# Performance work log

Hardware: AMD Instinct MI355X
Metric: run time of the kernel (lower is better)

## Reference

```python
import jax, jax.numpy as jnp
import numpy as np

N, E, B, D = 50000, 1600000, 256, 64


def _lin(k, fan_in, fan_out):
    kw, kb = jax.random.split(k)
    bound = 1.0 / np.sqrt(fan_in)
    w = jax.random.uniform(kw, (fan_in, fan_out), jnp.float32, -bound, bound)
    b = jax.random.uniform(kb, (fan_out,), jnp.float32, -bound, bound)
    return w, b


def setup_inputs() -> dict:
    key = jax.random.key(0)
    ks = jax.random.split(key, 16)
    inp = {
        "x": jax.random.normal(ks[0], (N, D), jnp.float32),
        "edge_attr": jax.random.normal(ks[1], (E, D), jnp.float32),
        "u": jax.random.normal(ks[2], (B, D), jnp.float32),
        "edge_index": jax.random.randint(ks[3], (2, E), 0, N, jnp.int32),
        "batch": jnp.sort(jax.random.randint(ks[4], (N,), 0, B, jnp.int32)),
    }
    # three MLPs: edge (in 4D), node (in 3D), global (in 3D); dims [2D, 2D, D]
    specs = [("e", 4 * D), ("n", 3 * D), ("g", 3 * D)]
    ki = 5
    for name, in_dim in specs:
        dims = [in_dim, 2 * D, 2 * D, D]
        for li in range(3):
            w, b = _lin(ks[ki], dims[li], dims[li + 1]); ki += 1
            inp[f"{name}w{li+1}"] = w
            inp[f"{name}b{li+1}"] = b
    return inp


def _mlp(h, w1, b1, w2, b2, w3, b3):
    h = h @ w1 + b1
    h = jax.nn.relu(h) @ w2 + b2
    h = jax.nn.relu(h) @ w3 + b3
    return h


def _scatter_mean(src, idx, num_segments):
    s = jax.ops.segment_sum(src, idx, num_segments=num_segments)
    c = jax.ops.segment_sum(jnp.ones_like(src[:, :1]), idx, num_segments=num_segments)
    return s / jnp.maximum(c, 1.0)


def reference(x, edge_attr, u,
              ew1, eb1, ew2, eb2, ew3, eb3,
              nw1, nb1, nw2, nb2, nw3, nb3,
              gw1, gb1, gw2, gb2, gw3, gb3,
              edge_index, batch):
    row, col = edge_index[0], edge_index[1]
    # edge model: cat[src, dest, edge_attr, u[batch[row]]] -> MLP
    e_in = jnp.concatenate([x[row], x[col], edge_attr, u[batch[row]]], axis=1)  # [E, 4D]
    e = _mlp(e_in, ew1, eb1, ew2, eb2, ew3, eb3)  # [E, D]
    # node model: scatter_mean(edge_attr', row) cat x cat u[batch] -> MLP
    n_agg = _scatter_mean(e, row, x.shape[0])  # [N, D]
    n_in = jnp.concatenate([n_agg, x, u[batch]], axis=1)  # [N, 3D]
    xn = _mlp(n_in, nw1, nb1, nw2, nb2, nw3, nb3)  # [N, D]
    # global model: cat[u, scatter_mean(x', batch), scatter_mean(e', batch[row])]
    edge_mean = _scatter_mean(e, batch[row], u.shape[0])  # [B, D]
    node_mean = _scatter_mean(xn, batch, u.shape[0])  # [B, D]
    g_in = jnp.concatenate([u, node_mean, edge_mean], axis=1)  # [B, 3D]
    un = _mlp(g_in, gw1, gb1, gw2, gb2, gw3, gb3)  # [B, D]
    return xn, e, un
```

## Files before the change

### kernel.cpp

```cpp
#include <hip/hip_runtime.h>

#define NN 50000
#define EE 1600000
#define BBATCH 256
#define DD 64

typedef _Float16 f16;
typedef _Float16 f16x4 __attribute__((ext_vector_type(4)));
typedef _Float16 f16x8 __attribute__((ext_vector_type(8)));
typedef float f32x4 __attribute__((ext_vector_type(4)));

#define MFMA16(a,b,c) __builtin_amdgcn_mfma_f32_16x16x32_f16((a),(b),(c),0,0,0)

constexpr int EW1_RL  = 264;
constexpr int EW1_OFF = 0;
constexpr int EW2_OFF = EW1_OFF + 128 * EW1_RL;
constexpr int EW3_OFF = EW2_OFF + 128 * 136;
constexpr int EH_OFF  = EW3_OFF + 64 * 136;
constexpr int EB_OFF  = EH_OFF + 8 * 16 * 72;
constexpr int ELDS    = EB_OFF + 640;

constexpr int NW1_RL  = 200;
constexpr int NW1_OFF = 0;
constexpr int NW2_OFF = NW1_OFF + 128 * NW1_RL;
constexpr int NW3_OFF = NW2_OFF + 128 * 136;
constexpr int NH_OFF  = NW3_OFF + 64 * 136;
constexpr int NB_OFF  = NH_OFF + 4 * 32 * 136;
constexpr int NLDS    = NB_OFF + 640;

__device__ __forceinline__ f16x8 pack8(const float* __restrict__ p) {
  f32x4 a = *(const f32x4*)p;
  f32x4 b = *(const f32x4*)(p + 4);
  f16x8 r;
  r[0]=(f16)a[0]; r[1]=(f16)a[1]; r[2]=(f16)a[2]; r[3]=(f16)a[3];
  r[4]=(f16)b[0]; r[5]=(f16)b[1]; r[6]=(f16)b[2]; r[7]=(f16)b[3];
  return r;
}
__device__ __forceinline__ f16x8 pack8s(const float* __restrict__ p, float sc) {
  f32x4 a = *(const f32x4*)p;
  f32x4 b = *(const f32x4*)(p + 4);
  a = a * sc; b = b * sc;
  f16x8 r;
  r[0]=(f16)a[0]; r[1]=(f16)a[1]; r[2]=(f16)a[2]; r[3]=(f16)a[3];
  r[4]=(f16)b[0]; r[5]=(f16)b[1]; r[6]=(f16)b[2]; r[7]=(f16)b[3];
  return r;
}
__device__ __forceinline__ f16x8 cvt8(f32x4 a, f32x4 b) {
  f16x8 r;
  r[0]=(f16)a[0]; r[1]=(f16)a[1]; r[2]=(f16)a[2]; r[3]=(f16)a[3];
  r[4]=(f16)b[0]; r[5]=(f16)b[1]; r[6]=(f16)b[2]; r[7]=(f16)b[3];
  return r;
}

template<int KSL, int W1RL, int W1O, int W2O, int W3O>
__device__ __forceinline__ void mlp3_core(f16* __restrict__ sm,
    const float* __restrict__ b1l, const float* __restrict__ b2l,
    const float* __restrict__ b3l,
    const f16x8 (&A1)[2][KSL], const int hb, const int r15, const int g,
    f32x4 (&acc3)[2][4])
{
  #pragma unroll
  for (int hh = 0; hh < 2; ++hh) {
    f32x4 acc[2][4];
    #pragma unroll
    for (int nt = 0; nt < 4; ++nt) {
      const float bv = b1l[(hh*4 + nt)*16 + r15];
      acc[0][nt] = (f32x4){bv, bv, bv, bv};
      acc[1][nt] = acc[0][nt];
    }
    #pragma unroll
    for (int s = 0; s < KSL; ++s) {
      #pragma unroll
      for (int nt = 0; nt < 4; ++nt) {
        const f16x8 bf = *(const f16x8*)&sm[W1O + ((hh*4+nt)*16 + r15) * W1RL + s*32 + g*8];
        acc[0][nt] = MFMA16(A1[0][s], bf, acc[0][nt]);
        acc[1][nt] = MFMA16(A1[1][s], bf, acc[1][nt]);
      }
    }
    #pragma unroll
    for (int mt = 0; mt < 2; ++mt)
      #pragma unroll
      for (int nt = 0; nt < 4; ++nt)
        #pragma unroll
        for (int i = 0; i < 4; ++i)
          sm[hb + (mt*16 + g*4 + i)*136 + (hh*4+nt)*16 + r15] =
              (f16)fmaxf(acc[mt][nt][i], 0.f);
  }

  f16x8 A2[2][4];
  #pragma unroll
  for (int mt = 0; mt < 2; ++mt)
    #pragma unroll
    for (int s = 0; s < 4; ++s)
      A2[mt][s] = *(const f16x8*)&sm[hb + (mt*16 + r15)*136 + s*32 + g*8];

  #pragma unroll
  for (int hh = 0; hh < 2; ++hh) {
    f32x4 acc[2][4];
    #pragma unroll
    for (int nt = 0; nt < 4; ++nt) {
      const float bv = b2l[(hh*4 + nt)*16 + r15];
      acc[0][nt] = (f32x4){bv, bv, bv, bv};
      acc[1][nt] = acc[0][nt];
    }
    #pragma unroll
    for (int s = 0; s < 4; ++s) {
      #pragma unroll
      for (int nt = 0; nt < 4; ++nt) {
        const f16x8 bf = *(const f16x8*)&sm[W2O + ((hh*4+nt)*16 + r15)*136 + s*32 + g*8];
        acc[0][nt] = MFMA16(A2[0][s], bf, acc[0][nt]);
        acc[1][nt] = MFMA16(A2[1][s], bf, acc[1][nt]);
      }
    }
    #pragma unroll
    for (int mt = 0; mt < 2; ++mt)
      #pragma unroll
      for (int nt = 0; nt < 4; ++nt)
        #pragma unroll
        for (int i = 0; i < 4; ++i)
          sm[hb + (mt*16 + g*4 + i)*136 + (hh*4+nt)*16 + r15] =
              (f16)fmaxf(acc[mt][nt][i], 0.f);
  }

  f16x8 A3[2][4];
  #pragma unroll
  for (int mt = 0; mt < 2; ++mt)
    #pragma unroll
    for (int s = 0; s < 4; ++s)
      A3[mt][s] = *(const f16x8*)&sm[hb + (mt*16 + r15)*136 + s*32 + g*8];

  #pragma unroll
  for (int nt = 0; nt < 4; ++nt) {
    const float bv = b3l[nt*16 + r15];
    acc3[0][nt] = (f32x4){bv, bv, bv, bv};
    acc3[1][nt] = acc3[0][nt];
  }
  #pragma unroll
  for (int s = 0; s < 4; ++s) {
    #pragma unroll
    for (int nt = 0; nt < 4; ++nt) {
      const f16x8 bf = *(const f16x8*)&sm[W3O + (nt*16 + r15)*136 + s*32 + g*8];
      acc3[0][nt] = MFMA16(A3[0][s], bf, acc3[0][nt]);
      acc3[1][nt] = MFMA16(A3[1][s], bf, acc3[1][nt]);
    }
  }
}

__global__ void transpose_all(
    const float* __restrict__ e1, const float* __restrict__ e2, const float* __restrict__ e3,
    const float* __restrict__ n1, const float* __restrict__ n2, const float* __restrict__ n3,
    const float* __restrict__ q1, const float* __restrict__ q2, const float* __restrict__ q3,
    f16* __restrict__ dst) {
  int tid = blockIdx.x * 256 + threadIdx.x;
  const int o1=32768,o2=49152,o3=57344,o4=81920,o5=98304,o6=106496,o7=131072,o8=147456,o9=155648;
  if (tid >= o9) return;
  const float* src; int in, od, rel;
  if      (tid < o1) { src=e1; in=256; od=128; rel=tid;    }
  else if (tid < o2) { src=e2; in=128; od=128; rel=tid-o1; }
  else if (tid < o3) { src=e3; in=128; od=64;  rel=tid-o2; }
  else if (tid < o4) { src=n1; in=192; od=128; rel=tid-o3; }
  else if (tid < o5) { src=n2; in=128; od=128; rel=tid-o4; }
  else if (tid < o6) { src=n3; in=128; od=64;  rel=tid-o5; }
  else if (tid < o7) { src=q1; in=192; od=128; rel=tid-o6; }
  else if (tid < o8) { src=q2; in=128; od=128; rel=tid-o7; }
  else               { src=q3; in=128; od=64;  rel=tid-o8; }
  int o = rel / in, i = rel - o * in;
  dst[tid] = (f16)src[(size_t)i * od + o];
}

__global__ void cvt_xu(const float* __restrict__ x, const float* __restrict__ u,
                       f16* __restrict__ xh, f16* __restrict__ uh) {
  const int XT = NN * 64 / 4;
  const int UT = BBATCH * 64 / 4;
  int tid = blockIdx.x * 256 + threadIdx.x;
  for (int i = tid; i < XT; i += gridDim.x * 256) {
    f32x4 v = *(const f32x4*)&x[(size_t)i * 4];
    f16x4 h; h[0]=(f16)v[0]; h[1]=(f16)v[1]; h[2]=(f16)v[2]; h[3]=(f16)v[3];
    *(f16x4*)&xh[(size_t)i * 4] = h;
  }
  if (tid < UT) {
    f32x4 v = *(const f32x4*)&u[(size_t)tid * 4];
    f16x4 h; h[0]=(f16)v[0]; h[1]=(f16)v[1]; h[2]=(f16)v[2]; h[3]=(f16)v[3];
    *(f16x4*)&uh[(size_t)tid * 4] = h;
  }
}

__global__ void count_kernel(const int* __restrict__ ei, int* __restrict__ deg) {
  int tid = blockIdx.x * 256 + threadIdx.x;
  if (tid < EE) atomicAdd(&deg[ei[tid]], 1);
}

__global__ __launch_bounds__(1024) void scan_kernel(const int* __restrict__ deg,
                                                    int* __restrict__ offs,
                                                    int* __restrict__ cursor) {
  const int t = threadIdx.x;
  const int per = (NN + 1023) / 1024;
  const int s0 = t * per;
  int s1 = s0 + per; if (s1 > NN) s1 = NN;
  int sum = 0;
  for (int i = s0; i < s1; ++i) sum += deg[i];
  const int lane = t & 63, wid = t >> 6;
  int v = sum;
  #pragma unroll
  for (int off = 1; off < 64; off <<= 1) {
    int o = __shfl_up(v, off);
    if (lane >= off) v += o;
  }
  __shared__ int wsums[16];
  __shared__ int wexcl[16];
  if (lane == 63) wsums[wid] = v;
  __syncthreads();
  if (t == 0) { int run = 0; for (int k = 0; k < 16; ++k) { wexcl[k] = run; run += wsums[k]; } }
  __syncthreads();
  int run = wexcl[wid] + v - sum;
  for (int i = s0; i < s1; ++i) { int d = deg[i]; offs[i] = run; cursor[i] = run; run += d; }
  if (t == 1023) offs[NN] = run;
}

__global__ void fill_kernel(const int* __restrict__ ei, int* __restrict__ cursor,
                            int* __restrict__ elist) {
  int tid = blockIdx.x * 256 + threadIdx.x;
  if (tid < EE) {
    int r = ei[tid];
    int pos = atomicAdd(&cursor[r], 1);
    elist[pos] = tid;
  }
}

__global__ __launch_bounds__(512, 2) void edge_mlp_kernel(
    const f16* __restrict__ xh, const float* __restrict__ ea,
    const f16* __restrict__ uh, const int* __restrict__ ei,
    const int* __restrict__ batch,
    const f16* __restrict__ w1t, const f16* __restrict__ w2t, const f16* __restrict__ w3t,
    const float* __restrict__ b1, const float* __restrict__ b2, const float* __restrict__ b3,
    float* __restrict__ e_out)
{
  __shared__ __align__(16) f16 sm[ELDS];
  const int t = threadIdx.x;
  for (int c = t; c < 4096; c += 512) { int r = c >> 5, kc = c & 31;
    *(uint4*)&sm[EW1_OFF + r*EW1_RL + kc*8] = *(const uint4*)&w1t[r*256 + kc*8]; }
  for (int c = t; c < 2048; c += 512) { int r = c >> 4, kc = c & 15;
    *(uint4*)&sm[EW2_OFF + r*136 + kc*8] = *(const uint4*)&w2t[r*128 + kc*8]; }
  for (int c = t; c < 1024; c += 512) { int r = c >> 4, kc = c & 15;
    *(uint4*)&sm[EW3_OFF + r*136 + kc*8] = *(const uint4*)&w3t[r*128 + kc*8]; }
  float* bias = (float*)&sm[EB_OFF];
  if (t < 128) { bias[t] = b1[t]; bias[128 + t] = b2[t]; }
  else if (t < 192) { bias[256 + (t - 128)] = b3[t - 128]; }
  __syncthreads();

  const int l = t & 63, w = t >> 6;
  const int r15 = l & 15, g = l >> 4;
  const int hb = EH_OFF + w * (16 * 72);
  const int NT = EE / 256;
  const int stride = gridDim.x;
  const int t0 = blockIdx.x;

  int rC[2], cC[2], bC[2];
  int rN[2], cN[2], bN[2];
  f16x8 Bx[2][6];
  f32x4 Gea[2][2][2];

  auto issueXU = [&](const int (&rr)[2], const int (&cc)[2], const int (&bb)[2]) {
    #pragma unroll
    for (int mt = 0; mt < 2; ++mt) {
      const f16* pr = xh + (size_t)rr[mt] * 64 + g * 8;
      const f16* pc = xh + (size_t)cc[mt] * 64 + g * 8;
      const f16* pu = uh + (size_t)bb[mt] * 64 + g * 8;
      Bx[mt][0] = *(const f16x8*)pr;        Bx[mt][1] = *(const f16x8*)(pr + 32);
      Bx[mt][2] = *(const f16x8*)pc;        Bx[mt][3] = *(const f16x8*)(pc + 32);
      Bx[mt][4] = *(const f16x8*)pu;        Bx[mt][5] = *(const f16x8*)(pu + 32);
    }
  };
  auto issueEA = [&](int tt) {
    #pragma unroll
    for (int mt = 0; mt < 2; ++mt) {
      const float* pe = ea + ((size_t)(tt * 256 + w * 32 + mt * 16 + r15)) * 64 + g * 8;
      #pragma unroll
      for (int ss = 0; ss < 2; ++ss) {
        Gea[mt][ss][0] = *(const f32x4*)(pe + ss * 32);
        Gea[mt][ss][1] = *(const f32x4*)(pe + ss * 32 + 4);
      }
    }
  };

  {
    int rr[2], cc[2], bb[2];
    #pragma unroll
    for (int mt = 0; mt < 2; ++mt) {
      const int eid = t0 * 256 + w * 32 + mt * 16 + r15;
      rr[mt] = ei[eid]; cc[mt] = ei[EE + eid];
    }
    #pragma unroll
    for (int mt = 0; mt < 2; ++mt) bb[mt] = batch[rr[mt]];
    issueXU(rr, cc, bb); issueEA(t0);
    int t1 = t0 + stride; if (t1 >= NT) t1 = t0;
    #pragma unroll
    for (int mt = 0; mt < 2; ++mt) {
      const int eid = t1 * 256 + w * 32 + mt * 16 + r15;
      rC[mt] = ei[eid]; cC[mt] = ei[EE + eid];
    }
    #pragma unroll
    for (int mt = 0; mt < 2; ++mt) bC[mt] = batch[rC[mt]];
  }

  for (int tile = t0; tile < NT; tile += stride) {
    f16x8 A[2][8];
    #pragma unroll
    for (int mt = 0; mt < 2; ++mt) {
      A[mt][0] = Bx[mt][0]; A[mt][1] = Bx[mt][1];
      A[mt][2] = Bx[mt][2]; A[mt][3] = Bx[mt][3];
      A[mt][4] = cvt8(Gea[mt][0][0], Gea[mt][0][1]);
      A[mt][5] = cvt8(Gea[mt][1][0], Gea[mt][1][1]);
      A[mt][6] = Bx[mt][4]; A[mt][7] = Bx[mt][5];
    }

    int t2 = tile + 2 * stride; if (t2 >= NT) t2 = t0;
    #pragma unroll
    for (int mt = 0; mt < 2; ++mt) {
      const int eid = t2 * 256 + w * 32 + mt * 16 + r15;
      rN[mt] = ei[eid]; cN[mt] = ei[EE + eid];
    }

    f32x4 acc1[2][8];
    #pragma unroll
    for (int a = 0; a < 8; ++a) {
      const f32x4 bv = *(const f32x4*)&bias[a*16 + g*4];
      acc1[0][a] = bv; acc1[1][a] = bv;
    }
    #pragma unroll
    for (int s = 0; s < 8; ++s)
      #pragma unroll
      for (int a = 0; a < 8; ++a) {
        const f16x8 wf = *(const f16x8*)&sm[EW1_OFF + (a*16 + r15)*EW1_RL + s*32 + g*8];
        acc1[0][a] = MFMA16(wf, A[0][s], acc1[0][a]);
        acc1[1][a] = MFMA16(wf, A[1][s], acc1[1][a]);
      }

    #pragma unroll
    for (int mt = 0; mt < 2; ++mt) bN[mt] = batch[rN[mt]];

    f16x8 B2[2][4];
    #pragma unroll
    for (int mt = 0; mt < 2; ++mt)
      #pragma unroll
      for (int hh = 0; hh < 2; ++hh) {
        #pragma unroll
        for (int ap = 0; ap < 4; ++ap) {
          const f32x4 v = acc1[mt][hh*4 + ap];
          f16x4 hv;
          hv[0]=(f16)fmaxf(v[0],0.f); hv[1]=(f16)fmaxf(v[1],0.f);
          hv[2]=(f16)fmaxf(v[2],0.f); hv[3]=(f16)fmaxf(v[3],0.f);
          *(f16x4*)&sm[hb + r15*72 + ap*16 + g*4] = hv;
        }
        #pragma unroll
        for (int sl = 0; sl < 2; ++sl)
          B2[mt][hh*2 + sl] = *(const f16x8*)&sm[hb + r15*72 + sl*32 + g*8];
      }

    int t1 = tile + stride; if (t1 >= NT) t1 = t0;
    issueXU(rC, cC, bC);

    f32x4 acc2[2][8];
    #pragma unroll
    for (int a = 0; a < 8; ++a) {
      const f32x4 bv = *(const f32x4*)&bias[128 + a*16 + g*4];
      acc2[0][a] = bv; acc2[1][a] = bv;
    }
    #pragma unroll
    for (int s = 0; s < 4; ++s)
      #pragma unroll
      for (int a = 0; a < 8; ++a) {
        const f16x8 wf = *(const f16x8*)&sm[EW2_OFF + (a*16 + r15)*136 + s*32 + g*8];
        acc2[0][a] = MFMA16(wf, B2[0][s], acc2[0][a]);
        acc2[1][a] = MFMA16(wf, B2[1][s], acc2[1][a]);
      }

    f16x8 B3[2][4];
    #pragma unroll
    for (int mt = 0; mt < 2; ++mt)
      #pragma unroll
      for (int hh = 0; hh < 2; ++hh) {
        #pragma unroll
        for (int ap = 0; ap < 4; ++ap) {
          const f32x4 v = acc2[mt][hh*4 + ap];
          f16x4 hv;
          hv[0]=(f16)fmaxf(v[0],0.f); hv[1]=(f16)fmaxf(v[1],0.f);
          hv[2]=(f16)fmaxf(v[2],0.f); hv[3]=(f16)fmaxf(v[3],0.f);
          *(f16x4*)&sm[hb + r15*72 + ap*16 + g*4] = hv;
        }
        #pragma unroll
        for (int sl = 0; sl < 2; ++sl)
          B3[mt][hh*2 + sl] = *(const f16x8*)&sm[hb + r15*72 + sl*32 + g*8];
      }

    issueEA(t1);

    f32x4 acc3[2][4];
    #pragma unroll
    for (int a = 0; a < 4; ++a) {
      const f32x4 bv = *(const f32x4*)&bias[256 + a*16 + g*4];
      acc3[0][a] = bv; acc3[1][a] = bv;
    }
    #pragma unroll
    for (int s = 0; s < 4; ++s)
      #pragma unroll
      for (int a = 0; a < 4; ++a) {
        const f16x8 wf = *(const f16x8*)&sm[EW3_OFF + (a*16 + r15)*136 + s*32 + g*8];
        acc3[0][a] = MFMA16(wf, B3[0][s], acc3[0][a]);
        acc3[1][a] = MFMA16(wf, B3[1][s], acc3[1][a]);
      }

    const int base = tile * 256 + w * 32;
    #pragma unroll
    for (int mt = 0; mt < 2; ++mt) {
      const int m = base + mt * 16 + r15;
      #pragma unroll
      for (int a = 0; a < 4; ++a)
        *(f32x4*)&e_out[(size_t)m * 64 + a*16 + g*4] = acc3[mt][a];
    }

    #pragma unroll
    for (int mt = 0; mt < 2; ++mt) { rC[mt] = rN[mt]; cC[mt] = cN[mt]; bC[mt] = bN[mt]; }
  }
}

__global__ void nsum_kernel(const float* __restrict__ e_src, const int* __restrict__ offs,
                            const int* __restrict__ elist, float* __restrict__ n_sum) {
  const int l = threadIdx.x & 63;
  const int wid = (blockIdx.x * blockDim.x + threadIdx.x) >> 6;
  const int nw = (gridDim.x * blockDim.x) >> 6;
  for (int node = wid; node < NN; node += nw) {
    const int s = offs[node], e = offs[node + 1];
    float acc = 0.f;
    int j = s;
    for (; j + 8 <= e; j += 8) {
      float v0 = e_src[(size_t)elist[j]   * 64 + l];
      float v1 = e_src[(size_t)elist[j+1] * 64 + l];
      float v2 = e_src[(size_t)elist[j+2] * 64 + l];
      float v3 = e_src[(size_t)elist[j+3] * 64 + l];
      float v4 = e_src[(size_t)elist[j+4] * 64 + l];
      float v5 = e_src[(size_t)elist[j+5] * 64 + l];
      float v6 = e_src[(size_t)elist[j+6] * 64 + l];
      float v7 = e_src[(size_t)elist[j+7] * 64 + l];
      acc += ((v0 + v1) + (v2 + v3)) + ((v4 + v5) + (v6 + v7));
    }
    for (; j < e; ++j) acc += e_src[(size_t)elist[j] * 64 + l];
    n_sum[(size_t)node * 64 + l] = acc;
  }
}

__global__ __launch_bounds__(256, 1) void node_mlp_kernel(
    const float* __restrict__ x, const float* __restrict__ u,
    const int* __restrict__ batch, const float* __restrict__ n_sum,
    const int* __restrict__ deg,
    const f16* __restrict__ w1t, const f16* __restrict__ w2t, const f16* __restrict__ w3t,
    const float* __restrict__ b1, const float* __restrict__ b2, const float* __restrict__ b3,
    float* __restrict__ xn_out)
{
  __shared__ __align__(16) f16 sm[NLDS];
  const int t = threadIdx.x;
  for (int c = t; c < 3072; c += 256) { int r = c / 24, kc = c - r * 24;
    *(uint4*)&sm[NW1_OFF + r*NW1_RL + kc*8] = *(const uint4*)&w1t[r*192 + kc*8]; }
  for (int c = t; c < 2048; c += 256) { int r = c >> 4, kc = c & 15;
    *(uint4*)&sm[NW2_OFF + r*136 + kc*8] = *(const uint4*)&w2t[r*128 + kc*8]; }
  for (int c = t; c < 1024; c += 256) { int r = c >> 4, kc = c & 15;
    *(uint4*)&sm[NW3_OFF + r*136 + kc*8] = *(const uint4*)&w3t[r*128 + kc*8]; }
  float* bias = (float*)&sm[NB_OFF];
  if (t < 128) { bias[t] = b1[t]; bias[128 + t] = b2[t]; }
  if (t < 64)  { bias[256 + t] = b3[t]; }
  __syncthreads();

  const int l = t & 63, w = t >> 6;
  const int r15 = l & 15, g = l >> 4;
  const int hb = NH_OFF + w * (32 * 136);
  const int NTT = (NN + 127) / 128;

  for (int tile = blockIdx.x; tile < NTT; tile += gridDim.x) {
    const int base = tile * 128 + w * 32;
    f16x8 A1[2][6];
    #pragma unroll
    for (int mt = 0; mt < 2; ++mt) {
      int raw = base + mt * 16 + r15;
      int node = raw < NN ? raw : NN - 1;
      float inv = 1.0f / fmaxf((float)deg[node], 1.0f);
      const float* sA = n_sum + (size_t)node * 64;
      const float* sB = x + (size_t)node * 64;
      const float* sC = u + (size_t)batch[node] * 64;
      #pragma unroll
      for (int s = 0; s < 6; ++s) {
        const int off = (s & 1) * 32 + g * 8;
        if (s < 2)      A1[mt][s] = pack8s(sA + off, inv);
        else if (s < 4) A1[mt][s] = pack8(sB + off);
        else            A1[mt][s] = pack8(sC + off);
      }
    }
    f32x4 acc3[2][4];
    mlp3_core<6, NW1_RL, NW1_OFF, NW2_OFF, NW3_OFF>(sm, bias, bias + 128, bias + 256,
                                                    A1, hb, r15, g, acc3);
    #pragma unroll
    for (int mt = 0; mt < 2; ++mt)
      #pragma unroll
      for (int nt = 0; nt < 4; ++nt)
        #pragma unroll
        for (int i = 0; i < 4; ++i) {
          const int m = base + mt * 16 + g * 4 + i;
          if (m < NN) xn_out[(size_t)m * 64 + nt * 16 + r15] = acc3[mt][nt][i];
        }
  }
}

__global__ void bstart_kernel(const int* __restrict__ batch, int* __restrict__ bstart) {
  int tid = blockIdx.x * 256 + threadIdx.x;
  if (tid >= NN) return;
  int b = batch[tid];
  if (tid == 0) { for (int k = 0; k <= b; ++k) bstart[k] = 0; }
  else { int pb = batch[tid - 1]; for (int k = pb + 1; k <= b; ++k) bstart[k] = tid; }
  if (tid == NN - 1) { for (int k = b + 1; k <= BBATCH; ++k) bstart[k] = NN; }
}

__global__ void batch_sum_kernel(const float* __restrict__ xn, const float* __restrict__ n_sum,
                                 const int* __restrict__ deg, const int* __restrict__ bstart,
                                 float* __restrict__ nbsum, float* __restrict__ ebsum,
                                 int* __restrict__ ncnt, int* __restrict__ ecnt) {
  __shared__ float red0[256];
  __shared__ float red1[256];
  __shared__ int   redi[256];
  const int b = blockIdx.x;
  const int s = bstart[b], e = bstart[b + 1];
  const int t = threadIdx.x, c = t & 63, j0 = t >> 6;
  float xs = 0.f, ns = 0.f; int dc = 0;
  for (int j = s + j0; j < e; j += 4) {
    xs += xn[(size_t)j * 64 + c];
    ns += n_sum[(size_t)j * 64 + c];
    if (c == 0) dc += deg[j];
  }
  red0[t] = xs; red1[t] = ns; redi[t] = dc;
  __syncthreads();
  if (t < 128) { red0[t] += red0[t + 128]; red1[t] += red1[t + 128]; redi[t] += redi[t + 128]; }
  __syncthreads();
  if (t < 64) {
    float a0 = red0[t] + red0[t + 64];
    float a1 = red1[t] + red1[t + 64];
    nbsum[b * 64 + t] = a0;
    ebsum[b * 64 + t] = a1;
    if (t == 0) { ncnt[b] = e - s; ecnt[b] = redi[0] + redi[64]; }
  }
}

__global__ __launch_bounds__(256, 1) void global_mlp_kernel(
    const float* __restrict__ u, const float* __restrict__ nbsum,
    const float* __restrict__ ebsum, const int* __restrict__ ncnt,
    const int* __restrict__ ecnt,
    const f16* __restrict__ w1t, const f16* __restrict__ w2t, const f16* __restrict__ w3t,
    const float* __restrict__ b1, const float* __restrict__ b2, const float* __restrict__ b3,
    float* __restrict__ un_out)
{
  __shared__ __align__(16) f16 sm[NLDS];
  const int t = threadIdx.x;
  for (int c = t; c < 3072; c += 256) { int r = c / 24, kc = c - r * 24;
    *(uint4*)&sm[NW1_OFF + r*NW1_RL + kc*8] = *(const uint4*)&w1t[r*192 + kc*8]; }
  for (int c = t; c < 2048; c += 256) { int r = c >> 4, kc = c & 15;
    *(uint4*)&sm[NW2_OFF + r*136 + kc*8] = *(const uint4*)&w2t[r*128 + kc*8]; }
  for (int c = t; c < 1024; c += 256) { int r = c >> 4, kc = c & 15;
    *(uint4*)&sm[NW3_OFF + r*136 + kc*8] = *(const uint4*)&w3t[r*128 + kc*8]; }
  float* bias = (float*)&sm[NB_OFF];
  if (t < 128) { bias[t] = b1[t]; bias[128 + t] = b2[t]; }
  if (t < 64)  { bias[256 + t] = b3[t]; }
  __syncthreads();

  const int l = t & 63, w = t >> 6;
  const int r15 = l & 15, g = l >> 4;
  const int hb = NH_OFF + w * (32 * 136);
  const int base = blockIdx.x * 128 + w * 32;

  f16x8 A1[2][6];
  #pragma unroll
  for (int mt = 0; mt < 2; ++mt) {
    const int r = base + mt * 16 + r15;
    const float invn = 1.0f / fmaxf((float)ncnt[r], 1.0f);
    const float inve = 1.0f / fmaxf((float)ecnt[r], 1.0f);
    const float* sA = u + (size_t)r * 64;
    const float* sB = nbsum + (size_t)r * 64;
    const float* sC = ebsum + (size_t)r * 64;
    #pragma unroll
    for (int s = 0; s < 6; ++s) {
      const int off = (s & 1) * 32 + g * 8;
      if (s < 2)      A1[mt][s] = pack8(sA + off);
      else if (s < 4) A1[mt][s] = pack8s(sB + off, invn);
      else            A1[mt][s] = pack8s(sC + off, inve);
    }
  }
  f32x4 acc3[2][4];
  mlp3_core<6, NW1_RL, NW1_OFF, NW2_OFF, NW3_OFF>(sm, bias, bias + 128, bias + 256,
                                                  A1, hb, r15, g, acc3);
  #pragma unroll
  for (int mt = 0; mt < 2; ++mt)
    #pragma unroll
    for (int nt = 0; nt < 4; ++nt)
      #pragma unroll
      for (int i = 0; i < 4; ++i) {
        const int m = base + mt * 16 + g * 4 + i;
        un_out[(size_t)m * 64 + nt * 16 + r15] = acc3[mt][nt][i];
      }
}

extern "C" void kernel_launch(void* const* d_in, const int* in_sizes, int n_in,
                              void* d_out, int out_size, void* d_ws, size_t ws_size,
                              hipStream_t stream)
{
  (void)in_sizes; (void)n_in; (void)out_size; (void)ws_size;
  const float* x     = (const float*)d_in[0];
  const float* ea    = (const float*)d_in[1];
  const float* u     = (const float*)d_in[2];
  const int*   ei    = (const int*)d_in[3];
  const int*   batch = (const int*)d_in[4];
  const float* ew1 = (const float*)d_in[5];  const float* eb1 = (const float*)d_in[6];
  const float* ew2 = (const float*)d_in[7];  const float* eb2 = (const float*)d_in[8];
  const float* ew3 = (const float*)d_in[9];  const float* eb3 = (const float*)d_in[10];
  const float* nw1 = (const float*)d_in[11]; const float* nb1 = (const float*)d_in[12];
  const float* nw2 = (const float*)d_in[13]; const float* nb2 = (const float*)d_in[14];
  const float* nw3 = (const float*)d_in[15]; const float* nb3 = (const float*)d_in[16];
  const float* gw1 = (const float*)d_in[17]; const float* gb1 = (const float*)d_in[18];
  const float* gw2 = (const float*)d_in[19]; const float* gb2 = (const float*)d_in[20];
  const float* gw3 = (const float*)d_in[21]; const float* gb3 = (const float*)d_in[22];

  float* xn_out = (float*)d_out;
  float* e_out  = xn_out + (size_t)NN * DD;
  float* un_out = e_out + (size_t)EE * DD;

  char* p = (char*)d_ws;
  auto alloc = [&](size_t bytes) -> void* {
    void* r = (void*)p; p += (bytes + 255) & ~(size_t)255; return r;
  };
  f16* wtE1 = (f16*)alloc(256 * 128 * 2);
  f16* wtE2 = (f16*)alloc(128 * 128 * 2);
  f16* wtE3 = (f16*)alloc(128 * 64 * 2);
  f16* wtN1 = (f16*)alloc(192 * 128 * 2);
  f16* wtN2 = (f16*)alloc(128 * 128 * 2);
  f16* wtN3 = (f16*)alloc(128 * 64 * 2);
  f16* wtG1 = (f16*)alloc(192 * 128 * 2);
  f16* wtG2 = (f16*)alloc(128 * 128 * 2);
  f16* wtG3 = (f16*)alloc(128 * 64 * 2);
  int* deg    = (int*)alloc((size_t)NN * 4);
  int* offs   = (int*)alloc((size_t)(NN + 1) * 4);
  int* cursor = (int*)alloc((size_t)NN * 4);
  int* elist  = (int*)alloc((size_t)EE * 4);
  int* bstart = (int*)alloc((size_t)(BBATCH + 1) * 4);
  float* nbsum = (float*)alloc((size_t)BBATCH * 64 * 4);
  float* ebsum = (float*)alloc((size_t)BBATCH * 64 * 4);
  int* ncnt = (int*)alloc((size_t)BBATCH * 4);
  int* ecnt = (int*)alloc((size_t)BBATCH * 4);
  float* n_sum = (float*)alloc((size_t)NN * 64 * 4);
  f16* xh = (f16*)alloc((size_t)NN * 64 * 2);
  f16* uh = (f16*)alloc((size_t)BBATCH * 64 * 2);

  transpose_all<<<dim3(608), dim3(256), 0, stream>>>(
      ew1, ew2, ew3, nw1, nw2, nw3, gw1, gw2, gw3, wtE1);
  cvt_xu<<<dim3(1024), dim3(256), 0, stream>>>(x, u, xh, uh);

  hipMemsetAsync(deg, 0, (size_t)NN * 4, stream);
  count_kernel<<<dim3(6250), dim3(256), 0, stream>>>(ei, deg);
  scan_kernel<<<dim3(1), dim3(1024), 0, stream>>>(deg, offs, cursor);
  fill_kernel<<<dim3(6250), dim3(256), 0, stream>>>(ei, cursor, elist);

  edge_mlp_kernel<<<dim3(256), dim3(512), 0, stream>>>(
      xh, ea, uh, ei, batch, wtE1, wtE2, wtE3, eb1, eb2, eb3, e_out);

  nsum_kernel<<<dim3(2048), dim3(256), 0, stream>>>(e_out, offs, elist, n_sum);

  node_mlp_kernel<<<dim3(128), dim3(256), 0, stream>>>(
      x, u, batch, n_sum, deg, wtN1, wtN2, wtN3, nb1, nb2, nb3, xn_out);

  bstart_kernel<<<dim3((NN + 255) / 256), dim3(256), 0, stream>>>(batch, bstart);
  batch_sum_kernel<<<dim3(BBATCH), dim3(256), 0, stream>>>(
      xn_out, n_sum, deg, bstart, nbsum, ebsum, ncnt, ecnt);

  global_mlp_kernel<<<dim3(2), dim3(256), 0, stream>>>(
      u, nbsum, ebsum, ncnt, ecnt, wtG1, wtG2, wtG3, gb1, gb2, gb3, un_out);
}
```

Measured before the change: 752.8 us.

## Fuse prep kernels, unroll nsum gather to 16, double nsum and node grids

Merges the weight transpose, x/u fp16 conversion, degree counting and batch-start computation into one prep kernel, removing three launches. The nsum gather loop now keeps 16 loads in flight with a 4-wide tail, and the nsum and node-MLP grids are doubled to raise parallelism. Risks are more register use in nsum and extra blocks in node_mlp, which has launch_bounds(256,1) and a large LDS footprint.

```diff
diff --git a/kernel.cpp b/kernel.cpp
--- a/kernel.cpp
+++ b/kernel.cpp
@@ -146,48 +146,55 @@
   }
 }
 
-__global__ void transpose_all(
+__global__ void prep_kernel(
     const float* __restrict__ e1, const float* __restrict__ e2, const float* __restrict__ e3,
     const float* __restrict__ n1, const float* __restrict__ n2, const float* __restrict__ n3,
     const float* __restrict__ q1, const float* __restrict__ q2, const float* __restrict__ q3,
-    f16* __restrict__ dst) {
-  int tid = blockIdx.x * 256 + threadIdx.x;
-  const int o1=32768,o2=49152,o3=57344,o4=81920,o5=98304,o6=106496,o7=131072,o8=147456,o9=155648;
-  if (tid >= o9) return;
-  const float* src; int in, od, rel;
-  if      (tid < o1) { src=e1; in=256; od=128; rel=tid;    }
-  else if (tid < o2) { src=e2; in=128; od=128; rel=tid-o1; }
-  else if (tid < o3) { src=e3; in=128; od=64;  rel=tid-o2; }
-  else if (tid < o4) { src=n1; in=192; od=128; rel=tid-o3; }
-  else if (tid < o5) { src=n2; in=128; od=128; rel=tid-o4; }
-  else if (tid < o6) { src=n3; in=128; od=64;  rel=tid-o5; }
-  else if (tid < o7) { src=q1; in=192; od=128; rel=tid-o6; }
-  else if (tid < o8) { src=q2; in=128; od=128; rel=tid-o7; }
-  else               { src=q3; in=128; od=64;  rel=tid-o8; }
-  int o = rel / in, i = rel - o * in;
-  dst[tid] = (f16)src[(size_t)i * od + o];
-}
-
-__global__ void cvt_xu(const float* __restrict__ x, const float* __restrict__ u,
-                       f16* __restrict__ xh, f16* __restrict__ uh) {
-  const int XT = NN * 64 / 4;
-  const int UT = BBATCH * 64 / 4;
-  int tid = blockIdx.x * 256 + threadIdx.x;
-  for (int i = tid; i < XT; i += gridDim.x * 256) {
-    f32x4 v = *(const f32x4*)&x[(size_t)i * 4];
+    f16* __restrict__ wdst,
+    const float* __restrict__ x, const float* __restrict__ u,
+    f16* __restrict__ xh, f16* __restrict__ uh,
+    const int* __restrict__ ei, int* __restrict__ deg,
+    const int* __restrict__ batch, int* __restrict__ bstart)
+{
+  const int tid = blockIdx.x * 256 + threadIdx.x;
+
+  {
+    const int o1=32768,o2=49152,o3=57344,o4=81920,o5=98304,o6=106496,o7=131072,o8=147456,o9=155648;
+    if (tid < o9) {
+      const float* src; int in, od, rel;
+      if      (tid < o1) { src=e1; in=256; od=128; rel=tid;    }
+      else if (tid < o2) { src=e2; in=128; od=128; rel=tid-o1; }
+      else if (tid < o3) { src=e3; in=128; od=64;  rel=tid-o2; }
+      else if (tid < o4) { src=n1; in=192; od=128; rel=tid-o3; }
+      else if (tid < o5) { src=n2; in=128; od=128; rel=tid-o4; }
+      else if (tid < o6) { src=n3; in=128; od=64;  rel=tid-o5; }
+      else if (tid < o7) { src=q1; in=192; od=128; rel=tid-o6; }
+      else if (tid < o8) { src=q2; in=128; od=128; rel=tid-o7; }
+      else               { src=q3; in=128; od=64;  rel=tid-o8; }
+      int o = rel / in, i = rel - o * in;
+      wdst[tid] = (f16)src[(size_t)i * od + o];
+    }
+  }
+
+  if (tid < NN * 64 / 4) {
+    f32x4 v = *(const f32x4*)&x[(size_t)tid * 4];
     f16x4 h; h[0]=(f16)v[0]; h[1]=(f16)v[1]; h[2]=(f16)v[2]; h[3]=(f16)v[3];
-    *(f16x4*)&xh[(size_t)i * 4] = h;
-  }
-  if (tid < UT) {
+    *(f16x4*)&xh[(size_t)tid * 4] = h;
+  }
+  if (tid < BBATCH * 64 / 4) {
     f32x4 v = *(const f32x4*)&u[(size_t)tid * 4];
     f16x4 h; h[0]=(f16)v[0]; h[1]=(f16)v[1]; h[2]=(f16)v[2]; h[3]=(f16)v[3];
     *(f16x4*)&uh[(size_t)tid * 4] = h;
   }
-}
-
-__global__ void count_kernel(const int* __restrict__ ei, int* __restrict__ deg) {
-  int tid = blockIdx.x * 256 + threadIdx.x;
+
   if (tid < EE) atomicAdd(&deg[ei[tid]], 1);
+
+  if (tid < NN) {
+    int b = batch[tid];
+    if (tid == 0) { for (int k = 0; k <= b; ++k) bstart[k] = 0; }
+    else { int pb = batch[tid - 1]; for (int k = pb + 1; k <= b; ++k) bstart[k] = tid; }
+    if (tid == NN - 1) { for (int k = b + 1; k <= BBATCH; ++k) bstart[k] = NN; }
+  }
 }
 
 __global__ __launch_bounds__(1024) void scan_kernel(const int* __restrict__ deg,
@@ -433,16 +440,20 @@
     const int s = offs[node], e = offs[node + 1];
     float acc = 0.f;
     int j = s;
-    for (; j + 8 <= e; j += 8) {
+    for (; j + 16 <= e; j += 16) {
+      float v[16];
+      #pragma unroll
+      for (int k = 0; k < 16; ++k) v[k] = e_src[(size_t)elist[j + k] * 64 + l];
+      float s0 = ((v[0]+v[1])+(v[2]+v[3])) + ((v[4]+v[5])+(v[6]+v[7]));
+      float s1 = ((v[8]+v[9])+(v[10]+v[11])) + ((v[12]+v[13])+(v[14]+v[15]));
+      acc += s0 + s1;
+    }
+    for (; j + 4 <= e; j += 4) {
       float v0 = e_src[(size_t)elist[j]   * 64 + l];
       float v1 = e_src[(size_t)elist[j+1] * 64 + l];
       float v2 = e_src[(size_t)elist[j+2] * 64 + l];
       float v3 = e_src[(size_t)elist[j+3] * 64 + l];
-      float v4 = e_src[(size_t)elist[j+4] * 64 + l];
-      float v5 = e_src[(size_t)elist[j+5] * 64 + l];
-      float v6 = e_src[(size_t)elist[j+6] * 64 + l];
-      float v7 = e_src[(size_t)elist[j+7] * 64 + l];
-      acc += ((v0 + v1) + (v2 + v3)) + ((v4 + v5) + (v6 + v7));
+      acc += (v0 + v1) + (v2 + v3);
     }
     for (; j < e; ++j) acc += e_src[(size_t)elist[j] * 64 + l];
     n_sum[(size_t)node * 64 + l] = acc;
@@ -507,15 +518,6 @@
           if (m < NN) xn_out[(size_t)m * 64 + nt * 16 + r15] = acc3[mt][nt][i];
         }
   }
-}
-
-__global__ void bstart_kernel(const int* __restrict__ batch, int* __restrict__ bstart) {
-  int tid = blockIdx.x * 256 + threadIdx.x;
-  if (tid >= NN) return;
-  int b = batch[tid];
-  if (tid == 0) { for (int k = 0; k <= b; ++k) bstart[k] = 0; }
-  else { int pb = batch[tid - 1]; for (int k = pb + 1; k <= b; ++k) bstart[k] = tid; }
-  if (tid == NN - 1) { for (int k = b + 1; k <= BBATCH; ++k) bstart[k] = NN; }
 }
 
 __global__ void batch_sum_kernel(const float* __restrict__ xn, const float* __restrict__ n_sum,
@@ -654,24 +656,21 @@
   f16* xh = (f16*)alloc((size_t)NN * 64 * 2);
   f16* uh = (f16*)alloc((size_t)BBATCH * 64 * 2);
 
-  transpose_all<<<dim3(608), dim3(256), 0, stream>>>(
-      ew1, ew2, ew3, nw1, nw2, nw3, gw1, gw2, gw3, wtE1);
-  cvt_xu<<<dim3(1024), dim3(256), 0, stream>>>(x, u, xh, uh);
-
   hipMemsetAsync(deg, 0, (size_t)NN * 4, stream);
-  count_kernel<<<dim3(6250), dim3(256), 0, stream>>>(ei, deg);
+  prep_kernel<<<dim3(6250), dim3(256), 0, stream>>>(
+      ew1, ew2, ew3, nw1, nw2, nw3, gw1, gw2, gw3, wtE1,
+      x, u, xh, uh, ei, deg, batch, bstart);
   scan_kernel<<<dim3(1), dim3(1024), 0, stream>>>(deg, offs, cursor);
   fill_kernel<<<dim3(6250), dim3(256), 0, stream>>>(ei, cursor, elist);
 
   edge_mlp_kernel<<<dim3(256), dim3(512), 0, stream>>>(
       xh, ea, uh, ei, batch, wtE1, wtE2, wtE3, eb1, eb2, eb3, e_out);
 
-  nsum_kernel<<<dim3(2048), dim3(256), 0, stream>>>(e_out, offs, elist, n_sum);
-
-  node_mlp_kernel<<<dim3(128), dim3(256), 0, stream>>>(
+  nsum_kernel<<<dim3(4096), dim3(256), 0, stream>>>(e_out, offs, elist, n_sum);
+
+  node_mlp_kernel<<<dim3(256), dim3(256), 0, stream>>>(
       x, u, batch, n_sum, deg, wtN1, wtN2, wtN3, nb1, nb2, nb3, xn_out);
 
-  bstart_kernel<<<dim3((NN + 255) / 256), dim3(256), 0, stream>>>(batch, bstart);
   batch_sum_kernel<<<dim3(BBATCH), dim3(256), 0, stream>>>(
       xn_out, n_sum, deg, bstart, nbsum, ebsum, ncnt, ecnt);
 
```

Result: faster. 731.3 us (-2.9%).
